# Kernel tuning notes

Measured on AMD Instinct MI355X. Metric: run time of the kernel, lower is better.

Reference implementation:

```python
import jax, jax.numpy as jnp
import numpy as np

N, E, D, H, G, C = 50000, 800000, 3, 128, 64, 10

def setup_inputs() -> dict:
    key = jax.random.key(0)
    ks = jax.random.split(key, 10)
    s = 0.1  # small init scale
    return {
        "pos": jax.random.normal(ks[0], (N, D), jnp.float32),
        "edge_index": jax.random.randint(ks[1], (2, E), 0, N, dtype=jnp.int64),
        "batch": jnp.sort(jax.random.randint(ks[2], (N,), 0, G, dtype=jnp.int64)),
        "W1": jax.random.normal(ks[3], (D, H), jnp.float32) * s,
        "b1": jnp.zeros((H,), jnp.float32),
        "W2": jax.random.normal(ks[4], (H, H), jnp.float32) * s,
        "b2": jnp.zeros((H,), jnp.float32),
        "W3": jax.random.normal(ks[5], (H, H), jnp.float32) * s,
        "b3": jnp.zeros((H,), jnp.float32),
        "Wl1": jax.random.normal(ks[6], (H, H // 2), jnp.float32) * s,
        "bl1": jnp.zeros((H // 2,), jnp.float32),
        "Wl2": jax.random.normal(ks[7], (H // 2, C), jnp.float32) * s,
        "bl2": jnp.zeros((C,), jnp.float32),
        "num_graphs": G,
    }

def reference(pos, edge_index, batch, W1, b1, W2, b2, W3, b3, Wl1, bl1, Wl2, bl2, num_graphs):
    n = pos.shape[0]
    loop = jnp.arange(n, dtype=edge_index.dtype)
    # GCN: add self-loops, symmetric normalization deg^-1/2 (A+I) deg^-1/2
    src = jnp.concatenate([edge_index[0], loop])
    dst = jnp.concatenate([edge_index[1], loop])
    deg = jax.ops.segment_sum(jnp.ones(src.shape, pos.dtype), dst, num_segments=n)
    dinv = jax.lax.rsqrt(jnp.maximum(deg, 1e-12))  # deg >= 1 due to self-loops
    norm = dinv[src] * dinv[dst]  # [E+N]

    def gcn(x, W, b):
        h = x @ W                               # [N,F] dense transform first (PyG order)
        msg = h[src] * norm[:, None]            # gather + normalize
        return jax.ops.segment_sum(msg, dst, num_segments=n) + b  # scatter-add

    x = jax.nn.relu(gcn(pos, W1, b1))   # dropout = identity (eval mode)
    x = jax.nn.relu(gcn(x, W2, b2))
    x = jax.nn.relu(gcn(x, W3, b3))
    # global_mean_pool over batch ids
    sums = jax.ops.segment_sum(x, batch, num_segments=num_graphs)
    cnt = jax.ops.segment_sum(jnp.ones((n,), x.dtype), batch, num_segments=num_graphs)
    g = sums / jnp.maximum(cnt, 1.0)[:, None]   # [G,H]
    h = jax.nn.relu(g @ Wl1 + bl1)
    return h @ Wl2 + bl2
```

## Files before the change

### kernel.cpp

```cpp
#include <hip/hip_runtime.h>

#define H 128
#define LSTRIDE 136
#define PSTR 132
typedef unsigned int uint32;
typedef unsigned short ushort16;
typedef __attribute__((ext_vector_type(8))) short bf16x8;
typedef __attribute__((ext_vector_type(4))) float f32x4;

static __device__ __forceinline__ ushort16 f2bf(float f){
  uint32 u = __float_as_uint(f);
  uint32 r = (u + 0x7fff + ((u >> 16) & 1)) >> 16;
  return (ushort16)r;
}
static __device__ __forceinline__ float bflo(uint32 u){ return __uint_as_float(u << 16); }
static __device__ __forceinline__ float bfhi(uint32 u){ return __uint_as_float(u & 0xffff0000u); }

__global__ __launch_bounds__(256) void k_setup(int* __restrict__ deg, float* __restrict__ gsum,
                                               const int* __restrict__ batch, int n, int G,
                                               int* __restrict__ gb, int SB,
                                               const float* __restrict__ W2, const float* __restrict__ W3,
                                               ushort16* __restrict__ wp2, ushort16* __restrict__ wp3){
  int b = blockIdx.x;
  if (b < SB){
    int i = b*256 + threadIdx.x;
    if (i < n) deg[i] = 0;
    if (i < G*H) gsum[i] = 0.f;
    if (i <= G){
      int lo = 0, hi = n;
      while (lo < hi){ int m = (lo + hi) >> 1; if (batch[m] < i) lo = m + 1; else hi = m; }
      gb[i] = lo;
    }
  } else {
    int gid = (b - SB)*256 + threadIdx.x;
    const float* W = (gid < 2048) ? W2 : W3;
    ushort16* wp   = (gid < 2048) ? wp2 : wp3;
    int tid = gid & 2047;
    int frag = tid >> 6, lane = tid & 63;
    int kt = frag >> 3, ct = frag & 7;
    int m = lane & 15, quad = lane >> 4;
    const float* wrow = &W[(kt*32 + quad*8)*H + ct*16 + m];
    ushort16 vals[8];
    #pragma unroll
    for (int j = 0; j < 8; j++) vals[j] = f2bf(wrow[j*H]);
    uint4 o;
    o.x = (uint32)vals[0] | ((uint32)vals[1] << 16);
    o.y = (uint32)vals[2] | ((uint32)vals[3] << 16);
    o.z = (uint32)vals[4] | ((uint32)vals[5] << 16);
    o.w = (uint32)vals[6] | ((uint32)vals[7] << 16);
    *(uint4*)&wp[(size_t)tid*8] = o;
  }
}

__global__ __launch_bounds__(256) void k_count_rank(const int* __restrict__ dst, int E,
                                                    int* __restrict__ deg, unsigned short* __restrict__ rank){
  int i = blockIdx.x*256 + threadIdx.x;
  if (i < E) rank[i] = (unsigned short)atomicAdd(&deg[dst[i]], 1);
}

__global__ __launch_bounds__(256) void k_scan1(const int* __restrict__ deg, int n,
      int* __restrict__ offsets, int* __restrict__ bsum, float* __restrict__ dinv){
  __shared__ int sh[256];
  int b = blockIdx.x, t = threadIdx.x;
  int base = b*1024 + t*4;
  bool i0 = base+0 < n, i1 = base+1 < n, i2 = base+2 < n, i3 = base+3 < n;
  int d0=0,d1=0,d2=0,d3=0;
  if (i3){ int4 v = *(const int4*)&deg[base]; d0=v.x; d1=v.y; d2=v.z; d3=v.w; }
  else {
    if (i0) d0 = deg[base+0];
    if (i1) d1 = deg[base+1];
    if (i2) d2 = deg[base+2];
  }
  int e0 = i0? d0+1:0, e1 = i1? d1+1:0, e2 = i2? d2+1:0, e3 = i3? d3+1:0;
  sh[t] = e0+e1+e2+e3;
  __syncthreads();
  for (int off=1; off<256; off<<=1){
    int v = sh[t];
    int add = (t>=off)? sh[t-off] : 0;
    __syncthreads();
    sh[t] = v+add;
    __syncthreads();
  }
  int o0 = (t==0)?0:sh[t-1];
  int o1 = o0+e0, o2 = o1+e1, o3 = o2+e2;
  if (i0){ offsets[base+0]=o0; dinv[base+0]=rsqrtf((float)(d0+1)); }
  if (i1){ offsets[base+1]=o1; dinv[base+1]=rsqrtf((float)(d1+1)); }
  if (i2){ offsets[base+2]=o2; dinv[base+2]=rsqrtf((float)(d2+1)); }
  if (i3){ offsets[base+3]=o3; dinv[base+3]=rsqrtf((float)(d3+1)); }
  if (t==255) bsum[b] = sh[255];
}

__global__ __launch_bounds__(256) void k_scan3b(int* __restrict__ offsets, int n,
                                                const int* __restrict__ bsum, int B){
  __shared__ int sh[2];
  int b = blockIdx.x, t = threadIdx.x;
  if (t < 64){
    int v   = (t < B)? bsum[t] : 0;
    int pre = (t < b)? v : 0;
    int tot = v;
    for (int o=1; o<64; o<<=1){ pre += __shfl_xor(pre,o); tot += __shfl_xor(tot,o); }
    if (t == 0){ sh[0] = pre; sh[1] = tot; }
  }
  __syncthreads();
  int add = sh[0];
  int base = b*1024 + t*4;
  if (base+3 < n){
    int4 v = *(int4*)&offsets[base];
    v.x+=add; v.y+=add; v.z+=add; v.w+=add;
    *(int4*)&offsets[base] = v;
  } else {
    #pragma unroll
    for (int k=0;k<4;k++){ int i=base+k; if (i<n) offsets[i]+=add; }
  }
  if (b == B-1 && t == 255) offsets[n] = sh[1];
}

__global__ __launch_bounds__(256) void k_fill2(const int* __restrict__ src, const int* __restrict__ dst,
            int E, int n, const int* __restrict__ offsets, const unsigned short* __restrict__ rank,
            unsigned short* __restrict__ csr_src){
  int i = blockIdx.x*256 + threadIdx.x;
  if (i < E){
    csr_src[offsets[dst[i]] + 1 + rank[i]] = (unsigned short)src[i];
  } else if (i < E + n){
    int j = i - E;
    csr_src[offsets[j]] = (unsigned short)j;
  }
}

__global__ __launch_bounds__(256) void k_prescale(const float* __restrict__ pos, const float* __restrict__ dinv,
                                                  float4* __restrict__ y0, int n){
  int i = blockIdx.x*256 + threadIdx.x;
  if (i < n){
    float d = dinv[i];
    y0[i] = make_float4(pos[3*i]*d, pos[3*i+1]*d, pos[3*i+2]*d, 0.f);
  }
}

__global__ __launch_bounds__(256) void k_layer1(const float4* __restrict__ y0, const int* __restrict__ offsets,
      const unsigned short* __restrict__ csr_src, const float* __restrict__ dinv,
      const float* __restrict__ W1, const float* __restrict__ b1,
      ushort16* __restrict__ y1, int n){
  int node = blockIdx.x*256 + threadIdx.x;
  if (node >= n) return;
  int lo = offsets[node], hi = offsets[node+1];
  float x=0.f, y=0.f, z=0.f;
  int e = lo;
  for (; e+2 <= hi; e += 2){
    int s0 = csr_src[e], s1 = csr_src[e+1];
    float4 v0 = y0[s0], v1 = y0[s1];
    x += v0.x + v1.x; y += v0.y + v1.y; z += v0.z + v1.z;
  }
  if (e < hi){ float4 v = y0[csr_src[e]]; x += v.x; y += v.y; z += v.z; }
  float dn = dinv[node];
  x *= dn; y *= dn; z *= dn;
  ushort16* rowp = &y1[(size_t)node*H];
  for (int c8 = 0; c8 < 16; c8++){
    float4 wa0 = *(const float4*)&W1[c8*8];
    float4 wa1 = *(const float4*)&W1[c8*8+4];
    float4 wb0 = *(const float4*)&W1[H + c8*8];
    float4 wb1 = *(const float4*)&W1[H + c8*8+4];
    float4 wc0 = *(const float4*)&W1[2*H + c8*8];
    float4 wc1 = *(const float4*)&W1[2*H + c8*8+4];
    float4 bb0 = *(const float4*)&b1[c8*8];
    float4 bb1 = *(const float4*)&b1[c8*8+4];
    float o0 = fmaxf(x*wa0.x + y*wb0.x + z*wc0.x + bb0.x, 0.f) * dn;
    float o1 = fmaxf(x*wa0.y + y*wb0.y + z*wc0.y + bb0.y, 0.f) * dn;
    float o2 = fmaxf(x*wa0.z + y*wb0.z + z*wc0.z + bb0.z, 0.f) * dn;
    float o3 = fmaxf(x*wa0.w + y*wb0.w + z*wc0.w + bb0.w, 0.f) * dn;
    float o4 = fmaxf(x*wa1.x + y*wb1.x + z*wc1.x + bb1.x, 0.f) * dn;
    float o5 = fmaxf(x*wa1.y + y*wb1.y + z*wc1.y + bb1.y, 0.f) * dn;
    float o6 = fmaxf(x*wa1.z + y*wb1.z + z*wc1.z + bb1.z, 0.f) * dn;
    float o7 = fmaxf(x*wa1.w + y*wb1.w + z*wc1.w + bb1.w, 0.f) * dn;
    uint4 o;
    o.x = (uint32)f2bf(o0) | ((uint32)f2bf(o1) << 16);
    o.y = (uint32)f2bf(o2) | ((uint32)f2bf(o3) << 16);
    o.z = (uint32)f2bf(o4) | ((uint32)f2bf(o5) << 16);
    o.w = (uint32)f2bf(o6) | ((uint32)f2bf(o7) << 16);
    *(uint4*)&rowp[c8*8] = o;
  }
}

template<int POOL>
__global__ __launch_bounds__(256) void k_aggdense(const ushort16* __restrict__ y, const int* __restrict__ offsets,
      const unsigned short* __restrict__ csr_src, const float* __restrict__ dinv, const ushort16* __restrict__ wp,
      const float* __restrict__ bias,
      ushort16* __restrict__ yout, const int* __restrict__ batch, float* __restrict__ gsum, int n){
  __shared__ unsigned short As[16*LSTRIDE];
  __shared__ float pool[POOL ? 16*PSTR : 1];
  __shared__ unsigned short outs[POOL ? 1 : 16*PSTR];
  __shared__ int sbatch[POOL ? 16 : 1];
  int tid = threadIdx.x;
  int node16 = blockIdx.x*16;
  int nl = tid >> 4;
  int node = node16 + nl;
  int f8 = (tid & 15) * 8;

  if (POOL && tid < 16) sbatch[tid] = (node16 + tid < n) ? batch[node16 + tid] : -1;

  float a0=0,a1=0,a2=0,a3=0,a4=0,a5=0,a6=0,a7=0;
  float dn = 0.f;
  #define ADDU(u) { a0+=bflo(u.x); a1+=bfhi(u.x); a2+=bflo(u.y); a3+=bfhi(u.y); \
                    a4+=bflo(u.z); a5+=bfhi(u.z); a6+=bflo(u.w); a7+=bfhi(u.w); }
  if (node < n){
    int lo = offsets[node], hi = offsets[node+1];
    int e = lo;
    for (; e+8 <= hi; e += 8){
      int s0=csr_src[e],   s1=csr_src[e+1], s2=csr_src[e+2], s3=csr_src[e+3];
      int s4=csr_src[e+4], s5=csr_src[e+5], s6=csr_src[e+6], s7=csr_src[e+7];
      uint4 u0 = *(const uint4*)&y[(size_t)s0*H + f8];
      uint4 u1 = *(const uint4*)&y[(size_t)s1*H + f8];
      uint4 u2 = *(const uint4*)&y[(size_t)s2*H + f8];
      uint4 u3 = *(const uint4*)&y[(size_t)s3*H + f8];
      uint4 u4 = *(const uint4*)&y[(size_t)s4*H + f8];
      uint4 u5 = *(const uint4*)&y[(size_t)s5*H + f8];
      uint4 u6 = *(const uint4*)&y[(size_t)s6*H + f8];
      uint4 u7 = *(const uint4*)&y[(size_t)s7*H + f8];
      ADDU(u0); ADDU(u1); ADDU(u2); ADDU(u3);
      ADDU(u4); ADDU(u5); ADDU(u6); ADDU(u7);
    }
    for (; e < hi; e++){
      int s = csr_src[e];
      uint4 u = *(const uint4*)&y[(size_t)s*H + f8];
      ADDU(u);
    }
    dn = dinv[node];
  }
  #undef ADDU
  uint4 o;
  o.x = (uint32)f2bf(a0*dn) | ((uint32)f2bf(a1*dn) << 16);
  o.y = (uint32)f2bf(a2*dn) | ((uint32)f2bf(a3*dn) << 16);
  o.z = (uint32)f2bf(a4*dn) | ((uint32)f2bf(a5*dn) << 16);
  o.w = (uint32)f2bf(a6*dn) | ((uint32)f2bf(a7*dn) << 16);
  *(uint4*)&As[nl*LSTRIDE + f8] = o;
  __syncthreads();

  int wave = tid >> 6;
  int lane = tid & 63;
  int m = lane & 15, quad = lane >> 4;
  f32x4 acc0 = {0.f,0.f,0.f,0.f}, acc1 = {0.f,0.f,0.f,0.f};
  int ct0 = wave*2, ct1 = wave*2 + 1;
  #pragma unroll
  for (int kt = 0; kt < 4; kt++){
    bf16x8 af = *(const bf16x8*)&As[m*LSTRIDE + kt*32 + quad*8];
    bf16x8 b0 = *(const bf16x8*)&wp[(size_t)((kt*8+ct0)*64 + lane)*8];
    bf16x8 b1 = *(const bf16x8*)&wp[(size_t)((kt*8+ct1)*64 + lane)*8];
    acc0 = __builtin_amdgcn_mfma_f32_16x16x32_bf16(af, b0, acc0, 0, 0, 0);
    acc1 = __builtin_amdgcn_mfma_f32_16x16x32_bf16(af, b1, acc1, 0, 0, 0);
  }
  #pragma unroll
  for (int j = 0; j < 2; j++){
    int ct = wave*2 + j;
    int col = ct*16 + m;
    float bv = bias[col];
    f32x4 ac = j ? acc1 : acc0;
    #pragma unroll
    for (int r = 0; r < 4; r++){
      int rl = quad*4 + r;
      int orow = node16 + rl;
      if (orow < n){
        float v = fmaxf(ac[r] + bv, 0.f);
        if (POOL) pool[rl*PSTR + col] = v;
        else      outs[rl*PSTR + col] = f2bf(v * dinv[orow]);
      }
    }
  }
  __syncthreads();
  if (POOL){
    int col = tid & 127;
    int half = tid >> 7;
    float run = 0.f; int gprev = -1;
    for (int r = half*8; r < half*8 + 8; r++){
      int g = sbatch[r];
      if (g < 0) break;
      if (g != gprev){
        if (gprev >= 0) atomicAdd(&gsum[gprev*H + col], run);
        run = 0.f; gprev = g;
      }
      run += pool[r*PSTR + col];
    }
    if (gprev >= 0) atomicAdd(&gsum[gprev*H + col], run);
  } else {
    int row = tid >> 4;
    int orow = node16 + row;
    if (orow < n){
      const unsigned short* sp = &outs[row*PSTR + f8];
      uint4 v;
      v.x = (uint32)sp[0] | ((uint32)sp[1] << 16);
      v.y = (uint32)sp[2] | ((uint32)sp[3] << 16);
      v.z = (uint32)sp[4] | ((uint32)sp[5] << 16);
      v.w = (uint32)sp[6] | ((uint32)sp[7] << 16);
      *(uint4*)&yout[(size_t)orow*H + f8] = v;
    }
  }
}

__global__ __launch_bounds__(64) void k_head(const float* __restrict__ gsum, const int* __restrict__ gb,
            const float* __restrict__ Wl1, const float* __restrict__ bl1,
            const float* __restrict__ Wl2, const float* __restrict__ bl2,
            float* __restrict__ out){
  int g = blockIdx.x;
  int t = threadIdx.x;
  __shared__ float gs[H];
  __shared__ float h1[64];
  float inv = 1.f / fmaxf((float)(gb[g+1] - gb[g]), 1.f);
  gs[t]      = gsum[g*H + t]      * inv;
  gs[64 + t] = gsum[g*H + 64 + t] * inv;
  __syncthreads();
  float acc = bl1[t];
  for (int k = 0; k < H; k++) acc += gs[k] * Wl1[k*64 + t];
  h1[t] = fmaxf(acc, 0.f);
  __syncthreads();
  if (t < 10){
    float o = bl2[t];
    for (int j = 0; j < 64; j++) o += h1[j] * Wl2[j*10 + t];
    out[g*10 + t] = o;
  }
}

extern "C" void kernel_launch(void* const* d_in, const int* in_sizes, int n_in,
                              void* d_out, int out_size, void* d_ws, size_t ws_size,
                              hipStream_t stream){
  const float* pos = (const float*)d_in[0];
  const int*  ei   = (const int*)d_in[1];
  const int*  batch= (const int*)d_in[2];
  const float* W1 = (const float*)d_in[3];
  const float* b1 = (const float*)d_in[4];
  const float* W2 = (const float*)d_in[5];
  const float* b2 = (const float*)d_in[6];
  const float* W3 = (const float*)d_in[7];
  const float* b3 = (const float*)d_in[8];
  const float* Wl1 = (const float*)d_in[9];
  const float* bl1 = (const float*)d_in[10];
  const float* Wl2 = (const float*)d_in[11];
  const float* bl2 = (const float*)d_in[12];
  float* out = (float*)d_out;

  int N = in_sizes[0] / 3;
  int E = in_sizes[1] / 2;
  int G = out_size / 10;
  int B = (N + 1023) / 1024;
  int SB = (N + 255) / 256;

  char* p = (char*)d_ws;
  auto carve = [&](size_t bytes)->char* { char* q = p; p += (bytes + 255) & ~(size_t)255; return q; };
  int*            deg     = (int*)     carve(sizeof(int)    * (size_t)N);
  int*            offsets = (int*)     carve(sizeof(int)    * (size_t)(N+1));
  float*          dinv    = (float*)   carve(sizeof(float)  * (size_t)N);
  int*            bsum    = (int*)     carve(sizeof(int)    * 256);
  int*            gb      = (int*)     carve(sizeof(int)    * (size_t)(G+1));
  float*          gsum    = (float*)   carve(sizeof(float)  * (size_t)G * H);
  unsigned short* csr_src = (unsigned short*)carve(sizeof(unsigned short) * (size_t)(E+N));
  unsigned short* rank    = (unsigned short*)carve(sizeof(unsigned short) * (size_t)E);
  float4*         y0      = (float4*)  carve(sizeof(float4) * (size_t)N);
  ushort16*       ybufA   = (ushort16*)carve(sizeof(ushort16) * (size_t)N * H);
  ushort16*       ybufB   = (ushort16*)carve(sizeof(ushort16) * (size_t)N * H);
  ushort16*       wp2     = (ushort16*)carve(sizeof(ushort16) * 16384);
  ushort16*       wp3     = (ushort16*)carve(sizeof(ushort16) * 16384);

  const int* src = ei;
  const int* dst = ei + E;

  hipLaunchKernelGGL(k_setup, dim3(SB + 16), dim3(256), 0, stream,
                     deg, gsum, batch, N, G, gb, SB, W2, W3, wp2, wp3);

  hipLaunchKernelGGL(k_count_rank, dim3((E+255)/256),   dim3(256), 0, stream, dst, E, deg, rank);
  hipLaunchKernelGGL(k_scan1,      dim3(B),             dim3(256), 0, stream, deg, N, offsets, bsum, dinv);
  hipLaunchKernelGGL(k_scan3b,     dim3(B),             dim3(256), 0, stream, offsets, N, bsum, B);
  hipLaunchKernelGGL(k_fill2,      dim3((E+N+255)/256), dim3(256), 0, stream, src, dst, E, N, offsets, rank, csr_src);

  hipLaunchKernelGGL(k_prescale, dim3((N+255)/256), dim3(256), 0, stream, pos, dinv, y0, N);
  hipLaunchKernelGGL(k_layer1,   dim3((N+255)/256), dim3(256), 0, stream, y0, offsets, csr_src, dinv, W1, b1, ybufA, N);

  hipLaunchKernelGGL(k_aggdense<0>, dim3((N+15)/16), dim3(256), 0, stream,
                     ybufA, offsets, csr_src, dinv, wp2, b2, ybufB, (const int*)nullptr, (float*)nullptr, N);

  hipLaunchKernelGGL(k_aggdense<1>, dim3((N+15)/16), dim3(256), 0, stream,
                     ybufB, offsets, csr_src, dinv, wp3, b3, (ushort16*)nullptr, batch, gsum, N);

  hipLaunchKernelGGL(k_head, dim3(G), dim3(64), 0, stream, gsum, gb, Wl1, bl1, Wl2, bl2, out);
}
```

Baseline: 252.6 us.

## Fuse all GCN stages into one cooperative persistent kernel with grid syncs

Replaces the ten separate kernel launches with a single cooperative persistent kernel that moves between phases using grid-wide syncs. The two-pass block scan is replaced by wave-level scans that reserve their range through an atomic counter, so CSR row starts no longer follow node order. Row ends now come from start plus degree. This removes launch gaps and the extra scan pass, but the grid is capped at occupancy times CU count, which limits parallelism in the memory-bound gather phases and adds grid-barrier cost.

```diff
diff --git a/kernel.cpp b/kernel.cpp
--- a/kernel.cpp
+++ b/kernel.cpp
@@ -1,319 +1,291 @@
 #include <hip/hip_runtime.h>
+#include <hip/hip_cooperative_groups.h>
+
+namespace cg = cooperative_groups;
 
 #define H 128
 #define LSTRIDE 136
 #define PSTR 132
 typedef unsigned int uint32;
-typedef unsigned short ushort16;
+typedef unsigned short u16;
 typedef __attribute__((ext_vector_type(8))) short bf16x8;
 typedef __attribute__((ext_vector_type(4))) float f32x4;
 
-static __device__ __forceinline__ ushort16 f2bf(float f){
+static __device__ __forceinline__ u16 f2bf(float f){
   uint32 u = __float_as_uint(f);
   uint32 r = (u + 0x7fff + ((u >> 16) & 1)) >> 16;
-  return (ushort16)r;
+  return (u16)r;
 }
 static __device__ __forceinline__ float bflo(uint32 u){ return __uint_as_float(u << 16); }
 static __device__ __forceinline__ float bfhi(uint32 u){ return __uint_as_float(u & 0xffff0000u); }
 
-__global__ __launch_bounds__(256) void k_setup(int* __restrict__ deg, float* __restrict__ gsum,
-                                               const int* __restrict__ batch, int n, int G,
-                                               int* __restrict__ gb, int SB,
-                                               const float* __restrict__ W2, const float* __restrict__ W3,
-                                               ushort16* __restrict__ wp2, ushort16* __restrict__ wp3){
-  int b = blockIdx.x;
-  if (b < SB){
-    int i = b*256 + threadIdx.x;
-    if (i < n) deg[i] = 0;
-    if (i < G*H) gsum[i] = 0.f;
-    if (i <= G){
-      int lo = 0, hi = n;
-      while (lo < hi){ int m = (lo + hi) >> 1; if (batch[m] < i) lo = m + 1; else hi = m; }
-      gb[i] = lo;
-    }
-  } else {
-    int gid = (b - SB)*256 + threadIdx.x;
-    const float* W = (gid < 2048) ? W2 : W3;
-    ushort16* wp   = (gid < 2048) ? wp2 : wp3;
-    int tid = gid & 2047;
-    int frag = tid >> 6, lane = tid & 63;
+template<int POOL>
+static __device__ void aggdense_phase(const u16* __restrict__ y, const int* __restrict__ start,
+      const int* __restrict__ deg, const u16* __restrict__ csr, const float* __restrict__ dinv,
+      const u16* __restrict__ wp, const float* __restrict__ bias,
+      u16* __restrict__ yout, const int* __restrict__ batch, float* __restrict__ gsum, int n,
+      unsigned short* As, float* poolbuf, int* sbatch)
+{
+  int tid = threadIdx.x;
+  unsigned short* outs = (unsigned short*)poolbuf;
+  int ngrp = (n + 15) >> 4;
+  for (int grp = blockIdx.x; grp < ngrp; grp += gridDim.x){
+    int node16 = grp << 4;
+    int nl = tid >> 4;
+    int node = node16 + nl;
+    int f8 = (tid & 15) * 8;
+
+    float a0=0,a1=0,a2=0,a3=0,a4=0,a5=0,a6=0,a7=0;
+    float dn = 0.f;
+    #define ADDU(u) { a0+=bflo(u.x); a1+=bfhi(u.x); a2+=bflo(u.y); a3+=bfhi(u.y); \
+                      a4+=bflo(u.z); a5+=bfhi(u.z); a6+=bflo(u.w); a7+=bfhi(u.w); }
+    if (node < n){
+      int lo = start[node];
+      int hi = lo + deg[node] + 1;
+      int e = lo;
+      for (; e+8 <= hi; e += 8){
+        int s0=csr[e],   s1=csr[e+1], s2=csr[e+2], s3=csr[e+3];
+        int s4=csr[e+4], s5=csr[e+5], s6=csr[e+6], s7=csr[e+7];
+        uint4 u0 = *(const uint4*)&y[(size_t)s0*H + f8];
+        uint4 u1 = *(const uint4*)&y[(size_t)s1*H + f8];
+        uint4 u2 = *(const uint4*)&y[(size_t)s2*H + f8];
+        uint4 u3 = *(const uint4*)&y[(size_t)s3*H + f8];
+        uint4 u4 = *(const uint4*)&y[(size_t)s4*H + f8];
+        uint4 u5 = *(const uint4*)&y[(size_t)s5*H + f8];
+        uint4 u6 = *(const uint4*)&y[(size_t)s6*H + f8];
+        uint4 u7 = *(const uint4*)&y[(size_t)s7*H + f8];
+        ADDU(u0); ADDU(u1); ADDU(u2); ADDU(u3);
+        ADDU(u4); ADDU(u5); ADDU(u6); ADDU(u7);
+      }
+      for (; e < hi; e++){
+        int s = csr[e];
+        uint4 u = *(const uint4*)&y[(size_t)s*H + f8];
+        ADDU(u);
+      }
+      dn = dinv[node];
+    }
+    #undef ADDU
+    uint4 o;
+    o.x = (uint32)f2bf(a0*dn) | ((uint32)f2bf(a1*dn) << 16);
+    o.y = (uint32)f2bf(a2*dn) | ((uint32)f2bf(a3*dn) << 16);
+    o.z = (uint32)f2bf(a4*dn) | ((uint32)f2bf(a5*dn) << 16);
+    o.w = (uint32)f2bf(a6*dn) | ((uint32)f2bf(a7*dn) << 16);
+    *(uint4*)&As[nl*LSTRIDE + f8] = o;
+    __syncthreads();
+    if (POOL && tid < 16) sbatch[tid] = (node16 + tid < n) ? batch[node16 + tid] : -1;
+
+    int wave = tid >> 6;
+    int lane = tid & 63;
+    int m = lane & 15, quad = lane >> 4;
+    f32x4 acc0 = {0.f,0.f,0.f,0.f}, acc1 = {0.f,0.f,0.f,0.f};
+    int ct0 = wave*2, ct1 = wave*2 + 1;
+    #pragma unroll
+    for (int kt = 0; kt < 4; kt++){
+      bf16x8 af = *(const bf16x8*)&As[m*LSTRIDE + kt*32 + quad*8];
+      bf16x8 b0 = *(const bf16x8*)&wp[(size_t)((kt*8+ct0)*64 + lane)*8];
+      bf16x8 b1 = *(const bf16x8*)&wp[(size_t)((kt*8+ct1)*64 + lane)*8];
+      acc0 = __builtin_amdgcn_mfma_f32_16x16x32_bf16(af, b0, acc0, 0, 0, 0);
+      acc1 = __builtin_amdgcn_mfma_f32_16x16x32_bf16(af, b1, acc1, 0, 0, 0);
+    }
+    #pragma unroll
+    for (int j = 0; j < 2; j++){
+      int ct = wave*2 + j;
+      int col = ct*16 + m;
+      float bv = bias[col];
+      f32x4 ac = j ? acc1 : acc0;
+      #pragma unroll
+      for (int r = 0; r < 4; r++){
+        int rl = quad*4 + r;
+        int orow = node16 + rl;
+        if (orow < n){
+          float v = fmaxf(ac[r] + bv, 0.f);
+          if (POOL) poolbuf[rl*PSTR + col] = v;
+          else      outs[rl*PSTR + col] = f2bf(v * dinv[orow]);
+        }
+      }
+    }
+    __syncthreads();
+    if (POOL){
+      int col = tid & 127;
+      int half = tid >> 7;
+      float run = 0.f; int gprev = -1;
+      for (int r = half*8; r < half*8 + 8; r++){
+        int g = sbatch[r];
+        if (g < 0) break;
+        if (g != gprev){
+          if (gprev >= 0) atomicAdd(&gsum[gprev*H + col], run);
+          run = 0.f; gprev = g;
+        }
+        run += poolbuf[r*PSTR + col];
+      }
+      if (gprev >= 0) atomicAdd(&gsum[gprev*H + col], run);
+    } else {
+      int row = tid >> 4;
+      int orow = node16 + row;
+      if (orow < n){
+        const unsigned short* sp = &outs[row*PSTR + f8];
+        uint4 v;
+        v.x = (uint32)sp[0] | ((uint32)sp[1] << 16);
+        v.y = (uint32)sp[2] | ((uint32)sp[3] << 16);
+        v.z = (uint32)sp[4] | ((uint32)sp[5] << 16);
+        v.w = (uint32)sp[6] | ((uint32)sp[7] << 16);
+        *(uint4*)&yout[(size_t)orow*H + f8] = v;
+      }
+    }
+  }
+}
+
+__global__ __launch_bounds__(256, 4) void k_mega(
+    const float* __restrict__ pos, const int* __restrict__ ei, const int* __restrict__ batch,
+    const float* __restrict__ W1, const float* __restrict__ b1,
+    const float* __restrict__ W2, const float* __restrict__ b2,
+    const float* __restrict__ W3, const float* __restrict__ b3,
+    const float* __restrict__ Wl1, const float* __restrict__ bl1,
+    const float* __restrict__ Wl2, const float* __restrict__ bl2, float* __restrict__ out,
+    int n, int E, int G,
+    int* __restrict__ deg, u16* __restrict__ rank, int* __restrict__ start,
+    float* __restrict__ dinv, int* __restrict__ alloc_ctr,
+    int* __restrict__ gb, float* __restrict__ gsum, u16* __restrict__ csr, float4* __restrict__ y0,
+    u16* __restrict__ ybufA, u16* __restrict__ ybufB, u16* __restrict__ wp2, u16* __restrict__ wp3)
+{
+  __shared__ unsigned short As[16*LSTRIDE];
+  __shared__ float poolbuf[16*PSTR];
+  __shared__ int sbatch[16];
+  __shared__ float gs[H];
+  __shared__ float h1[64];
+
+  cg::grid_group gridg = cg::this_grid();
+  int tid = threadIdx.x;
+  int gtid = blockIdx.x*256 + tid;
+  int gstride = gridDim.x*256;
+  const int* src = ei;
+  const int* dst = ei + E;
+
+  for (int i = gtid; i < n; i += gstride) deg[i] = 0;
+  for (int i = gtid; i < G*H; i += gstride) gsum[i] = 0.f;
+  for (int g = gtid; g <= G; g += gstride){
+    int lo = 0, hi = n;
+    while (lo < hi){ int mm = (lo + hi) >> 1; if (batch[mm] < g) lo = mm + 1; else hi = mm; }
+    gb[g] = lo;
+  }
+  if (gtid == 0) *alloc_ctr = 0;
+  for (int g = gtid; g < 4096; g += gstride){
+    const float* W = (g < 2048) ? W2 : W3;
+    u16* wp = (g < 2048) ? wp2 : wp3;
+    int t2 = g & 2047;
+    int frag = t2 >> 6, lane = t2 & 63;
     int kt = frag >> 3, ct = frag & 7;
     int m = lane & 15, quad = lane >> 4;
     const float* wrow = &W[(kt*32 + quad*8)*H + ct*16 + m];
-    ushort16 vals[8];
+    u16 v[8];
     #pragma unroll
-    for (int j = 0; j < 8; j++) vals[j] = f2bf(wrow[j*H]);
+    for (int j = 0; j < 8; j++) v[j] = f2bf(wrow[j*H]);
     uint4 o;
-    o.x = (uint32)vals[0] | ((uint32)vals[1] << 16);
-    o.y = (uint32)vals[2] | ((uint32)vals[3] << 16);
-    o.z = (uint32)vals[4] | ((uint32)vals[5] << 16);
-    o.w = (uint32)vals[6] | ((uint32)vals[7] << 16);
-    *(uint4*)&wp[(size_t)tid*8] = o;
-  }
-}
-
-__global__ __launch_bounds__(256) void k_count_rank(const int* __restrict__ dst, int E,
-                                                    int* __restrict__ deg, unsigned short* __restrict__ rank){
-  int i = blockIdx.x*256 + threadIdx.x;
-  if (i < E) rank[i] = (unsigned short)atomicAdd(&deg[dst[i]], 1);
-}
-
-__global__ __launch_bounds__(256) void k_scan1(const int* __restrict__ deg, int n,
-      int* __restrict__ offsets, int* __restrict__ bsum, float* __restrict__ dinv){
-  __shared__ int sh[256];
-  int b = blockIdx.x, t = threadIdx.x;
-  int base = b*1024 + t*4;
-  bool i0 = base+0 < n, i1 = base+1 < n, i2 = base+2 < n, i3 = base+3 < n;
-  int d0=0,d1=0,d2=0,d3=0;
-  if (i3){ int4 v = *(const int4*)&deg[base]; d0=v.x; d1=v.y; d2=v.z; d3=v.w; }
-  else {
-    if (i0) d0 = deg[base+0];
-    if (i1) d1 = deg[base+1];
-    if (i2) d2 = deg[base+2];
-  }
-  int e0 = i0? d0+1:0, e1 = i1? d1+1:0, e2 = i2? d2+1:0, e3 = i3? d3+1:0;
-  sh[t] = e0+e1+e2+e3;
-  __syncthreads();
-  for (int off=1; off<256; off<<=1){
-    int v = sh[t];
-    int add = (t>=off)? sh[t-off] : 0;
-    __syncthreads();
-    sh[t] = v+add;
-    __syncthreads();
-  }
-  int o0 = (t==0)?0:sh[t-1];
-  int o1 = o0+e0, o2 = o1+e1, o3 = o2+e2;
-  if (i0){ offsets[base+0]=o0; dinv[base+0]=rsqrtf((float)(d0+1)); }
-  if (i1){ offsets[base+1]=o1; dinv[base+1]=rsqrtf((float)(d1+1)); }
-  if (i2){ offsets[base+2]=o2; dinv[base+2]=rsqrtf((float)(d2+1)); }
-  if (i3){ offsets[base+3]=o3; dinv[base+3]=rsqrtf((float)(d3+1)); }
-  if (t==255) bsum[b] = sh[255];
-}
-
-__global__ __launch_bounds__(256) void k_scan3b(int* __restrict__ offsets, int n,
-                                                const int* __restrict__ bsum, int B){
-  __shared__ int sh[2];
-  int b = blockIdx.x, t = threadIdx.x;
-  if (t < 64){
-    int v   = (t < B)? bsum[t] : 0;
-    int pre = (t < b)? v : 0;
-    int tot = v;
-    for (int o=1; o<64; o<<=1){ pre += __shfl_xor(pre,o); tot += __shfl_xor(tot,o); }
-    if (t == 0){ sh[0] = pre; sh[1] = tot; }
-  }
-  __syncthreads();
-  int add = sh[0];
-  int base = b*1024 + t*4;
-  if (base+3 < n){
-    int4 v = *(int4*)&offsets[base];
-    v.x+=add; v.y+=add; v.z+=add; v.w+=add;
-    *(int4*)&offsets[base] = v;
-  } else {
-    #pragma unroll
-    for (int k=0;k<4;k++){ int i=base+k; if (i<n) offsets[i]+=add; }
-  }
-  if (b == B-1 && t == 255) offsets[n] = sh[1];
-}
-
-__global__ __launch_bounds__(256) void k_fill2(const int* __restrict__ src, const int* __restrict__ dst,
-            int E, int n, const int* __restrict__ offsets, const unsigned short* __restrict__ rank,
-            unsigned short* __restrict__ csr_src){
-  int i = blockIdx.x*256 + threadIdx.x;
-  if (i < E){
-    csr_src[offsets[dst[i]] + 1 + rank[i]] = (unsigned short)src[i];
-  } else if (i < E + n){
-    int j = i - E;
-    csr_src[offsets[j]] = (unsigned short)j;
-  }
-}
-
-__global__ __launch_bounds__(256) void k_prescale(const float* __restrict__ pos, const float* __restrict__ dinv,
-                                                  float4* __restrict__ y0, int n){
-  int i = blockIdx.x*256 + threadIdx.x;
-  if (i < n){
-    float d = dinv[i];
-    y0[i] = make_float4(pos[3*i]*d, pos[3*i+1]*d, pos[3*i+2]*d, 0.f);
-  }
-}
-
-__global__ __launch_bounds__(256) void k_layer1(const float4* __restrict__ y0, const int* __restrict__ offsets,
-      const unsigned short* __restrict__ csr_src, const float* __restrict__ dinv,
-      const float* __restrict__ W1, const float* __restrict__ b1,
-      ushort16* __restrict__ y1, int n){
-  int node = blockIdx.x*256 + threadIdx.x;
-  if (node >= n) return;
-  int lo = offsets[node], hi = offsets[node+1];
-  float x=0.f, y=0.f, z=0.f;
-  int e = lo;
-  for (; e+2 <= hi; e += 2){
-    int s0 = csr_src[e], s1 = csr_src[e+1];
-    float4 v0 = y0[s0], v1 = y0[s1];
-    x += v0.x + v1.x; y += v0.y + v1.y; z += v0.z + v1.z;
-  }
-  if (e < hi){ float4 v = y0[csr_src[e]]; x += v.x; y += v.y; z += v.z; }
-  float dn = dinv[node];
-  x *= dn; y *= dn; z *= dn;
-  ushort16* rowp = &y1[(size_t)node*H];
-  for (int c8 = 0; c8 < 16; c8++){
-    float4 wa0 = *(const float4*)&W1[c8*8];
-    float4 wa1 = *(const float4*)&W1[c8*8+4];
-    float4 wb0 = *(const float4*)&W1[H + c8*8];
-    float4 wb1 = *(const float4*)&W1[H + c8*8+4];
-    float4 wc0 = *(const float4*)&W1[2*H + c8*8];
-    float4 wc1 = *(const float4*)&W1[2*H + c8*8+4];
-    float4 bb0 = *(const float4*)&b1[c8*8];
-    float4 bb1 = *(const float4*)&b1[c8*8+4];
-    float o0 = fmaxf(x*wa0.x + y*wb0.x + z*wc0.x + bb0.x, 0.f) * dn;
-    float o1 = fmaxf(x*wa0.y + y*wb0.y + z*wc0.y + bb0.y, 0.f) * dn;
-    float o2 = fmaxf(x*wa0.z + y*wb0.z + z*wc0.z + bb0.z, 0.f) * dn;
-    float o3 = fmaxf(x*wa0.w + y*wb0.w + z*wc0.w + bb0.w, 0.f) * dn;
-    float o4 = fmaxf(x*wa1.x + y*wb1.x + z*wc1.x + bb1.x, 0.f) * dn;
-    float o5 = fmaxf(x*wa1.y + y*wb1.y + z*wc1.y + bb1.y, 0.f) * dn;
-    float o6 = fmaxf(x*wa1.z + y*wb1.z + z*wc1.z + bb1.z, 0.f) * dn;
-    float o7 = fmaxf(x*wa1.w + y*wb1.w + z*wc1.w + bb1.w, 0.f) * dn;
-    uint4 o;
-    o.x = (uint32)f2bf(o0) | ((uint32)f2bf(o1) << 16);
-    o.y = (uint32)f2bf(o2) | ((uint32)f2bf(o3) << 16);
-    o.z = (uint32)f2bf(o4) | ((uint32)f2bf(o5) << 16);
-    o.w = (uint32)f2bf(o6) | ((uint32)f2bf(o7) << 16);
-    *(uint4*)&rowp[c8*8] = o;
-  }
-}
-
-template<int POOL>
-__global__ __launch_bounds__(256) void k_aggdense(const ushort16* __restrict__ y, const int* __restrict__ offsets,
-      const unsigned short* __restrict__ csr_src, const float* __restrict__ dinv, const ushort16* __restrict__ wp,
-      const float* __restrict__ bias,
-      ushort16* __restrict__ yout, const int* __restrict__ batch, float* __restrict__ gsum, int n){
-  __shared__ unsigned short As[16*LSTRIDE];
-  __shared__ float pool[POOL ? 16*PSTR : 1];
-  __shared__ unsigned short outs[POOL ? 1 : 16*PSTR];
-  __shared__ int sbatch[POOL ? 16 : 1];
-  int tid = threadIdx.x;
-  int node16 = blockIdx.x*16;
-  int nl = tid >> 4;
-  int node = node16 + nl;
-  int f8 = (tid & 15) * 8;
-
-  if (POOL && tid < 16) sbatch[tid] = (node16 + tid < n) ? batch[node16 + tid] : -1;
-
-  float a0=0,a1=0,a2=0,a3=0,a4=0,a5=0,a6=0,a7=0;
-  float dn = 0.f;
-  #define ADDU(u) { a0+=bflo(u.x); a1+=bfhi(u.x); a2+=bflo(u.y); a3+=bfhi(u.y); \
-                    a4+=bflo(u.z); a5+=bfhi(u.z); a6+=bflo(u.w); a7+=bfhi(u.w); }
-  if (node < n){
-    int lo = offsets[node], hi = offsets[node+1];
+    o.x = (uint32)v[0] | ((uint32)v[1] << 16);
+    o.y = (uint32)v[2] | ((uint32)v[3] << 16);
+    o.z = (uint32)v[4] | ((uint32)v[5] << 16);
+    o.w = (uint32)v[6] | ((uint32)v[7] << 16);
+    *(uint4*)&wp[(size_t)t2*8] = o;
+  }
+  gridg.sync();
+
+  for (int i = gtid; i < E; i += gstride) rank[i] = (u16)atomicAdd(&deg[dst[i]], 1);
+  gridg.sync();
+
+  {
+    int lane = tid & 63;
+    for (int i = gtid; (i - lane) < n; i += gstride){
+      int d = (i < n) ? deg[i] + 1 : 0;
+      int pre = d;
+      #pragma unroll
+      for (int o = 1; o < 64; o <<= 1){
+        int v = __shfl_up(pre, o);
+        if (lane >= o) pre += v;
+      }
+      int tot = __shfl(pre, 63);
+      int base = 0;
+      if (lane == 63 && tot > 0) base = atomicAdd(alloc_ctr, tot);
+      base = __shfl(base, 63);
+      if (i < n){
+        start[i] = base + pre - d;
+        float dv = rsqrtf((float)d);
+        dinv[i] = dv;
+        y0[i] = make_float4(pos[3*i]*dv, pos[3*i+1]*dv, pos[3*i+2]*dv, 0.f);
+      }
+    }
+  }
+  gridg.sync();
+
+  for (int i = gtid; i < E + n; i += gstride){
+    if (i < E) csr[start[dst[i]] + 1 + rank[i]] = (u16)src[i];
+    else { int j = i - E; csr[start[j]] = (u16)j; }
+  }
+  gridg.sync();
+
+  for (int node = gtid; node < n; node += gstride){
+    int lo = start[node], hi = lo + deg[node] + 1;
+    float x=0.f, y=0.f, z=0.f;
     int e = lo;
-    for (; e+8 <= hi; e += 8){
-      int s0=csr_src[e],   s1=csr_src[e+1], s2=csr_src[e+2], s3=csr_src[e+3];
-      int s4=csr_src[e+4], s5=csr_src[e+5], s6=csr_src[e+6], s7=csr_src[e+7];
-      uint4 u0 = *(const uint4*)&y[(size_t)s0*H + f8];
-      uint4 u1 = *(const uint4*)&y[(size_t)s1*H + f8];
-      uint4 u2 = *(const uint4*)&y[(size_t)s2*H + f8];
-      uint4 u3 = *(const uint4*)&y[(size_t)s3*H + f8];
-      uint4 u4 = *(const uint4*)&y[(size_t)s4*H + f8];
-      uint4 u5 = *(const uint4*)&y[(size_t)s5*H + f8];
-      uint4 u6 = *(const uint4*)&y[(size_t)s6*H + f8];
-      uint4 u7 = *(const uint4*)&y[(size_t)s7*H + f8];
-      ADDU(u0); ADDU(u1); ADDU(u2); ADDU(u3);
-      ADDU(u4); ADDU(u5); ADDU(u6); ADDU(u7);
-    }
-    for (; e < hi; e++){
-      int s = csr_src[e];
-      uint4 u = *(const uint4*)&y[(size_t)s*H + f8];
-      ADDU(u);
-    }
-    dn = dinv[node];
-  }
-  #undef ADDU
-  uint4 o;
-  o.x = (uint32)f2bf(a0*dn) | ((uint32)f2bf(a1*dn) << 16);
-  o.y = (uint32)f2bf(a2*dn) | ((uint32)f2bf(a3*dn) << 16);
-  o.z = (uint32)f2bf(a4*dn) | ((uint32)f2bf(a5*dn) << 16);
-  o.w = (uint32)f2bf(a6*dn) | ((uint32)f2bf(a7*dn) << 16);
-  *(uint4*)&As[nl*LSTRIDE + f8] = o;
-  __syncthreads();
-
-  int wave = tid >> 6;
-  int lane = tid & 63;
-  int m = lane & 15, quad = lane >> 4;
-  f32x4 acc0 = {0.f,0.f,0.f,0.f}, acc1 = {0.f,0.f,0.f,0.f};
-  int ct0 = wave*2, ct1 = wave*2 + 1;
-  #pragma unroll
-  for (int kt = 0; kt < 4; kt++){
-    bf16x8 af = *(const bf16x8*)&As[m*LSTRIDE + kt*32 + quad*8];
-    bf16x8 b0 = *(const bf16x8*)&wp[(size_t)((kt*8+ct0)*64 + lane)*8];
-    bf16x8 b1 = *(const bf16x8*)&wp[(size_t)((kt*8+ct1)*64 + lane)*8];
-    acc0 = __builtin_amdgcn_mfma_f32_16x16x32_bf16(af, b0, acc0, 0, 0, 0);
-    acc1 = __builtin_amdgcn_mfma_f32_16x16x32_bf16(af, b1, acc1, 0, 0, 0);
-  }
-  #pragma unroll
-  for (int j = 0; j < 2; j++){
-    int ct = wave*2 + j;
-    int col = ct*16 + m;
-    float bv = bias[col];
-    f32x4 ac = j ? acc1 : acc0;
-    #pragma unroll
-    for (int r = 0; r < 4; r++){
-      int rl = quad*4 + r;
-      int orow = node16 + rl;
-      if (orow < n){
-        float v = fmaxf(ac[r] + bv, 0.f);
-        if (POOL) pool[rl*PSTR + col] = v;
-        else      outs[rl*PSTR + col] = f2bf(v * dinv[orow]);
-      }
-    }
-  }
-  __syncthreads();
-  if (POOL){
-    int col = tid & 127;
-    int half = tid >> 7;
-    float run = 0.f; int gprev = -1;
-    for (int r = half*8; r < half*8 + 8; r++){
-      int g = sbatch[r];
-      if (g < 0) break;
-      if (g != gprev){
-        if (gprev >= 0) atomicAdd(&gsum[gprev*H + col], run);
-        run = 0.f; gprev = g;
-      }
-      run += pool[r*PSTR + col];
-    }
-    if (gprev >= 0) atomicAdd(&gsum[gprev*H + col], run);
-  } else {
-    int row = tid >> 4;
-    int orow = node16 + row;
-    if (orow < n){
-      const unsigned short* sp = &outs[row*PSTR + f8];
-      uint4 v;
-      v.x = (uint32)sp[0] | ((uint32)sp[1] << 16);
-      v.y = (uint32)sp[2] | ((uint32)sp[3] << 16);
-      v.z = (uint32)sp[4] | ((uint32)sp[5] << 16);
-      v.w = (uint32)sp[6] | ((uint32)sp[7] << 16);
-      *(uint4*)&yout[(size_t)orow*H + f8] = v;
-    }
-  }
-}
-
-__global__ __launch_bounds__(64) void k_head(const float* __restrict__ gsum, const int* __restrict__ gb,
-            const float* __restrict__ Wl1, const float* __restrict__ bl1,
-            const float* __restrict__ Wl2, const float* __restrict__ bl2,
-            float* __restrict__ out){
-  int g = blockIdx.x;
-  int t = threadIdx.x;
-  __shared__ float gs[H];
-  __shared__ float h1[64];
-  float inv = 1.f / fmaxf((float)(gb[g+1] - gb[g]), 1.f);
-  gs[t]      = gsum[g*H + t]      * inv;
-  gs[64 + t] = gsum[g*H + 64 + t] * inv;
-  __syncthreads();
-  float acc = bl1[t];
-  for (int k = 0; k < H; k++) acc += gs[k] * Wl1[k*64 + t];
-  h1[t] = fmaxf(acc, 0.f);
-  __syncthreads();
-  if (t < 10){
-    float o = bl2[t];
-    for (int j = 0; j < 64; j++) o += h1[j] * Wl2[j*10 + t];
-    out[g*10 + t] = o;
+    for (; e+2 <= hi; e += 2){
+      int s0 = csr[e], s1 = csr[e+1];
+      float4 v0 = y0[s0], v1 = y0[s1];
+      x += v0.x + v1.x; y += v0.y + v1.y; z += v0.z + v1.z;
+    }
+    if (e < hi){ float4 v = y0[csr[e]]; x += v.x; y += v.y; z += v.z; }
+    float dn = dinv[node];
+    x *= dn; y *= dn; z *= dn;
+    u16* rowp = &ybufA[(size_t)node*H];
+    for (int c8 = 0; c8 < 16; c8++){
+      float4 wa0 = *(const float4*)&W1[c8*8];
+      float4 wa1 = *(const float4*)&W1[c8*8+4];
+      float4 wb0 = *(const float4*)&W1[H + c8*8];
+      float4 wb1 = *(const float4*)&W1[H + c8*8+4];
+      float4 wc0 = *(const float4*)&W1[2*H + c8*8];
+      float4 wc1 = *(const float4*)&W1[2*H + c8*8+4];
+      float4 bb0 = *(const float4*)&b1[c8*8];
+      float4 bb1 = *(const float4*)&b1[c8*8+4];
+      float o0 = fmaxf(x*wa0.x + y*wb0.x + z*wc0.x + bb0.x, 0.f) * dn;
+      float o1 = fmaxf(x*wa0.y + y*wb0.y + z*wc0.y + bb0.y, 0.f) * dn;
+      float o2 = fmaxf(x*wa0.z + y*wb0.z + z*wc0.z + bb0.z, 0.f) * dn;
+      float o3 = fmaxf(x*wa0.w + y*wb0.w + z*wc0.w + bb0.w, 0.f) * dn;
+      float o4 = fmaxf(x*wa1.x + y*wb1.x + z*wc1.x + bb1.x, 0.f) * dn;
+      float o5 = fmaxf(x*wa1.y + y*wb1.y + z*wc1.y + bb1.y, 0.f) * dn;
+      float o6 = fmaxf(x*wa1.z + y*wb1.z + z*wc1.z + bb1.z, 0.f) * dn;
+      float o7 = fmaxf(x*wa1.w + y*wb1.w + z*wc1.w + bb1.w, 0.f) * dn;
+      uint4 o;
+      o.x = (uint32)f2bf(o0) | ((uint32)f2bf(o1) << 16);
+      o.y = (uint32)f2bf(o2) | ((uint32)f2bf(o3) << 16);
+      o.z = (uint32)f2bf(o4) | ((uint32)f2bf(o5) << 16);
+      o.w = (uint32)f2bf(o6) | ((uint32)f2bf(o7) << 16);
+      *(uint4*)&rowp[c8*8] = o;
+    }
+  }
+  gridg.sync();
+
+  aggdense_phase<0>(ybufA, start, deg, csr, dinv, wp2, b2, ybufB, (const int*)nullptr, (float*)nullptr, n,
+                    As, poolbuf, sbatch);
+  gridg.sync();
+
+  aggdense_phase<1>(ybufB, start, deg, csr, dinv, wp3, b3, (u16*)nullptr, batch, gsum, n,
+                    As, poolbuf, sbatch);
+  gridg.sync();
+
+  for (int g = blockIdx.x; g < G; g += gridDim.x){
+    float inv = 1.f / fmaxf((float)(gb[g+1] - gb[g]), 1.f);
+    if (tid < H) gs[tid] = gsum[g*H + tid] * inv;
+    __syncthreads();
+    if (tid < 64){
+      float acc = bl1[tid];
+      for (int k = 0; k < H; k++) acc += gs[k] * Wl1[k*64 + tid];
+      h1[tid] = fmaxf(acc, 0.f);
+    }
+    __syncthreads();
+    if (tid < 10){
+      float o = bl2[tid];
+      for (int j = 0; j < 64; j++) o += h1[j] * Wl2[j*10 + tid];
+      out[g*10 + tid] = o;
+    }
+    __syncthreads();
   }
 }
 
@@ -338,44 +310,46 @@
   int N = in_sizes[0] / 3;
   int E = in_sizes[1] / 2;
   int G = out_size / 10;
-  int B = (N + 1023) / 1024;
-  int SB = (N + 255) / 256;
 
   char* p = (char*)d_ws;
   auto carve = [&](size_t bytes)->char* { char* q = p; p += (bytes + 255) & ~(size_t)255; return q; };
-  int*            deg     = (int*)     carve(sizeof(int)    * (size_t)N);
-  int*            offsets = (int*)     carve(sizeof(int)    * (size_t)(N+1));
-  float*          dinv    = (float*)   carve(sizeof(float)  * (size_t)N);
-  int*            bsum    = (int*)     carve(sizeof(int)    * 256);
-  int*            gb      = (int*)     carve(sizeof(int)    * (size_t)(G+1));
-  float*          gsum    = (float*)   carve(sizeof(float)  * (size_t)G * H);
-  unsigned short* csr_src = (unsigned short*)carve(sizeof(unsigned short) * (size_t)(E+N));
-  unsigned short* rank    = (unsigned short*)carve(sizeof(unsigned short) * (size_t)E);
-  float4*         y0      = (float4*)  carve(sizeof(float4) * (size_t)N);
-  ushort16*       ybufA   = (ushort16*)carve(sizeof(ushort16) * (size_t)N * H);
-  ushort16*       ybufB   = (ushort16*)carve(sizeof(ushort16) * (size_t)N * H);
-  ushort16*       wp2     = (ushort16*)carve(sizeof(ushort16) * 16384);
-  ushort16*       wp3     = (ushort16*)carve(sizeof(ushort16) * 16384);
-
-  const int* src = ei;
-  const int* dst = ei + E;
-
-  hipLaunchKernelGGL(k_setup, dim3(SB + 16), dim3(256), 0, stream,
-                     deg, gsum, batch, N, G, gb, SB, W2, W3, wp2, wp3);
-
-  hipLaunchKernelGGL(k_count_rank, dim3((E+255)/256),   dim3(256), 0, stream, dst, E, deg, rank);
-  hipLaunchKernelGGL(k_scan1,      dim3(B),             dim3(256), 0, stream, deg, N, offsets, bsum, dinv);
-  hipLaunchKernelGGL(k_scan3b,     dim3(B),             dim3(256), 0, stream, offsets, N, bsum, B);
-  hipLaunchKernelGGL(k_fill2,      dim3((E+N+255)/256), dim3(256), 0, stream, src, dst, E, N, offsets, rank, csr_src);
-
-  hipLaunchKernelGGL(k_prescale, dim3((N+255)/256), dim3(256), 0, stream, pos, dinv, y0, N);
-  hipLaunchKernelGGL(k_layer1,   dim3((N+255)/256), dim3(256), 0, stream, y0, offsets, csr_src, dinv, W1, b1, ybufA, N);
-
-  hipLaunchKernelGGL(k_aggdense<0>, dim3((N+15)/16), dim3(256), 0, stream,
-                     ybufA, offsets, csr_src, dinv, wp2, b2, ybufB, (const int*)nullptr, (float*)nullptr, N);
-
-  hipLaunchKernelGGL(k_aggdense<1>, dim3((N+15)/16), dim3(256), 0, stream,
-                     ybufB, offsets, csr_src, dinv, wp3, b3, (ushort16*)nullptr, batch, gsum, N);
-
-  hipLaunchKernelGGL(k_head, dim3(G), dim3(64), 0, stream, gsum, gb, Wl1, bl1, Wl2, bl2, out);
+  int*    deg       = (int*)   carve(sizeof(int)    * (size_t)N);
+  u16*    rank      = (u16*)   carve(sizeof(u16)    * (size_t)E);
+  int*    start     = (int*)   carve(sizeof(int)    * (size_t)N);
+  float*  dinv      = (float*) carve(sizeof(float)  * (size_t)N);
+  int*    alloc_ctr = (int*)   carve(sizeof(int)    * 64);
+  int*    gb        = (int*)   carve(sizeof(int)    * (size_t)(G+1));
+  float*  gsum      = (float*) carve(sizeof(float)  * (size_t)G * H);
+  u16*    csr       = (u16*)   carve(sizeof(u16)    * (size_t)(E+N));
+  float4* y0        = (float4*)carve(sizeof(float4) * (size_t)N);
+  u16*    ybufA     = (u16*)   carve(sizeof(u16)    * (size_t)N * H);
+  u16*    ybufB     = (u16*)   carve(sizeof(u16)    * (size_t)N * H);
+  u16*    wp2       = (u16*)   carve(sizeof(u16)    * 16384);
+  u16*    wp3       = (u16*)   carve(sizeof(u16)    * 16384);
+
+  int maxb = 0;
+  if (hipOccupancyMaxActiveBlocksPerMultiprocessor(&maxb, (const void*)k_mega, 256, 0) != hipSuccess || maxb < 1)
+    maxb = 4;
+  int dev = 0;
+  hipGetDevice(&dev);
+  hipDeviceProp_t prop;
+  int cus = 256;
+  if (hipGetDeviceProperties(&prop, dev) == hipSuccess && prop.multiProcessorCount > 0)
+    cus = prop.multiProcessorCount;
+  long long gridll = (long long)maxb * cus;
+  if (gridll > 2048) gridll = 2048;
+  if (gridll < 64)   gridll = 64;
+  unsigned grid = (unsigned)gridll;
+
+  void* kargs[] = {
+    (void*)&pos, (void*)&ei, (void*)&batch,
+    (void*)&W1, (void*)&b1, (void*)&W2, (void*)&b2,
+    (void*)&W3, (void*)&b3, (void*)&Wl1, (void*)&bl1,
+    (void*)&Wl2, (void*)&bl2, (void*)&out,
+    (void*)&N, (void*)&E, (void*)&G,
+    (void*)&deg, (void*)&rank, (void*)&start, (void*)&dinv, (void*)&alloc_ctr,
+    (void*)&gb, (void*)&gsum, (void*)&csr, (void*)&y0,
+    (void*)&ybufA, (void*)&ybufB, (void*)&wp2, (void*)&wp3
+  };
+  hipLaunchCooperativeKernel((const void*)k_mega, dim3(grid), dim3(256), kargs, 0, stream);
 }
```

New measurement: 677.5 us. 2.68x slower.
